# Optimization experiments

Hardware: AMD Instinct MI355X
Metric: run time of the kernel (lower is better)

Reference implementation:

```python
import jax, jax.numpy as jnp
import numpy as np

B, T, I, H, O = 512, 1024, 15, 64, 11

def setup_inputs() -> dict:
    key = jax.random.key(0)
    ks = jax.random.split(key, 7)
    s_ih = 1.0 / np.sqrt(H)
    return {
        "x": jax.random.normal(ks[0], (B, T, I), dtype=jnp.float32),
        # torch nn.RNN params: weight_ih_l0 [H,I], weight_hh_l0 [H,H], biases [H]
        "W_ih": jax.random.uniform(ks[1], (H, I), jnp.float32, -s_ih, s_ih),
        "b_ih": jax.random.uniform(ks[2], (H,), jnp.float32, -s_ih, s_ih),
        "W_hh": jax.random.uniform(ks[3], (H, H), jnp.float32, -s_ih, s_ih),
        "b_hh": jax.random.uniform(ks[4], (H,), jnp.float32, -s_ih, s_ih),
        # decoder Linear(64, 11)
        "W_dec": jax.random.uniform(ks[5], (O, H), jnp.float32, -s_ih, s_ih),
        "b_dec": jax.random.uniform(ks[6], (O,), jnp.float32, -s_ih, s_ih),
    }

def reference(x, W_ih, b_ih, W_hh, b_hh, W_dec, b_dec):
    # Precompute input projection for all timesteps: [T, B, H]
    xproj = jnp.einsum("bti,hi->tbh", x, W_ih) + b_ih + b_hh
    h0 = jnp.zeros((x.shape[0], W_hh.shape[0]), dtype=x.dtype)

    def step(h, xp_t):
        h_new = jax.nn.relu(xp_t + h @ W_hh.T)  # [B, H]
        return h_new, h_new

    h_last, hs = jax.lax.scan(step, h0, xproj)  # hs: [T, B, H]
    out_seq = jnp.transpose(hs, (1, 0, 2))       # [B, T, H]
    out = jax.nn.relu(jnp.einsum("bth,oh->bto", out_seq, W_dec) + b_dec)
    h = h_last[None]  # [1, B, H] matching torch num_layers dim
    return (out, h)
```

## Files before the change

kernel.cpp:

```cpp
#include <hip/hip_runtime.h>
#include <hip/hip_fp16.h>
#include <stdint.h>

#define BB 512
#define TT 1024
#define II 15
#define HH 64
#define OO 11

typedef __fp16 half2v __attribute__((ext_vector_type(2)));
typedef _Float16 half8 __attribute__((ext_vector_type(8)));
typedef float floatx4 __attribute__((ext_vector_type(4)));
typedef int int4v __attribute__((ext_vector_type(4)));

union PK { int i; half2v h; float f; };

__device__ __forceinline__ half2v i2h2(int v) { PK u; u.i = v; return u.h; }
__device__ __forceinline__ int h22i(half2v v) { PK u; u.h = v; return u.i; }

__device__ __forceinline__ float FDOT2(half2v a, half2v b, float c) {
    return __builtin_amdgcn_fdot2(a, b, c, false);
}

__device__ __forceinline__ float lane_xor1(float v) {
    PK u; u.f = v;
    u.i = __builtin_amdgcn_mov_dpp(u.i, 0xB1, 0xF, 0xF, false);
    return u.f;
}

__global__ __launch_bounds__(64) void rnn_rec(
    const float* __restrict__ x, const float* __restrict__ W_ih,
    const float* __restrict__ b_ih, const float* __restrict__ W_hh,
    const float* __restrict__ b_hh, _Float16* __restrict__ hs,
    float* __restrict__ h_last)
{
    __shared__ __align__(16) int xbuf[64 * 8];
    __shared__ __align__(16) int hbuf[64];
    const int b = blockIdx.x;
    const int lane = threadIdx.x;

    half2v whh[32];
#pragma unroll
    for (int j = 0; j < 32; ++j)
        whh[j] = __builtin_amdgcn_cvt_pkrtz(W_hh[lane * HH + 2 * j],
                                            W_hh[lane * HH + 2 * j + 1]);
    half2v wx[8];
#pragma unroll
    for (int j = 0; j < 7; ++j)
        wx[j] = __builtin_amdgcn_cvt_pkrtz(W_ih[lane * II + 2 * j],
                                           W_ih[lane * II + 2 * j + 1]);
    wx[7] = __builtin_amdgcn_cvt_pkrtz(W_ih[lane * II + 14],
                                       b_ih[lane] + b_hh[lane]);

    const float* xb = x + (size_t)b * TT * II;
    _Float16* hrow = hs + (size_t)b * TT * HH + lane;
    const int hwslot = (lane >> 1) | ((lane & 1) << 5);

    {
        float cf[II];
#pragma unroll
        for (int i = 0; i < II; ++i) cf[i] = xb[lane * II + i];
        int4v p0, p1;
        p0.x = h22i(__builtin_amdgcn_cvt_pkrtz(cf[0], cf[1]));
        p0.y = h22i(__builtin_amdgcn_cvt_pkrtz(cf[2], cf[3]));
        p0.z = h22i(__builtin_amdgcn_cvt_pkrtz(cf[4], cf[5]));
        p0.w = h22i(__builtin_amdgcn_cvt_pkrtz(cf[6], cf[7]));
        p1.x = h22i(__builtin_amdgcn_cvt_pkrtz(cf[8], cf[9]));
        p1.y = h22i(__builtin_amdgcn_cvt_pkrtz(cf[10], cf[11]));
        p1.z = h22i(__builtin_amdgcn_cvt_pkrtz(cf[12], cf[13]));
        p1.w = h22i(__builtin_amdgcn_cvt_pkrtz(cf[14], 1.0f));
        *(int4v*)&xbuf[lane * 8] = p0;
        *(int4v*)&xbuf[lane * 8 + 4] = p1;
    }

    float h = 0.0f;

    for (int tc = 0; tc < TT; tc += 64) {
        const int tnb = (tc + 64 < TT) ? (tc + 64) : tc;
        float nf[II];
#pragma unroll
        for (int i = 0; i < II; ++i)
            nf[i] = xb[(size_t)(tnb + lane) * II + i];

#pragma unroll 4
        for (int ts = 0; ts < 64; ++ts) {
            PK hp;
            hp.h = __builtin_amdgcn_cvt_pkrtz(h, lane_xor1(h));
            hbuf[hwslot] = hp.i;

            const int4v xv0 = *(const int4v*)&xbuf[ts * 8];
            const int4v xv1 = *(const int4v*)&xbuf[ts * 8 + 4];
            int4v hb[8];
#pragma unroll
            for (int q = 0; q < 8; ++q)
                hb[q] = *(const int4v*)&hbuf[q * 4];

            float a0 = FDOT2(i2h2(xv0.x), wx[0], 0.0f);
            float a1 = FDOT2(i2h2(xv0.y), wx[1], 0.0f);
            float a2 = FDOT2(i2h2(xv0.z), wx[2], 0.0f);
            float a3 = FDOT2(i2h2(xv0.w), wx[3], 0.0f);
            a0 = FDOT2(i2h2(xv1.x), wx[4], a0);
            a1 = FDOT2(i2h2(xv1.y), wx[5], a1);
            a2 = FDOT2(i2h2(xv1.z), wx[6], a2);
            a3 = FDOT2(i2h2(xv1.w), wx[7], a3);
#pragma unroll
            for (int q = 0; q < 8; ++q) {
                a0 = FDOT2(i2h2(hb[q].x), whh[4 * q + 0], a0);
                a1 = FDOT2(i2h2(hb[q].y), whh[4 * q + 1], a1);
                a2 = FDOT2(i2h2(hb[q].z), whh[4 * q + 2], a2);
                a3 = FDOT2(i2h2(hb[q].w), whh[4 * q + 3], a3);
            }
            h = fmaxf((a0 + a1) + (a2 + a3), 0.0f);
            *hrow = (_Float16)h;
            hrow += HH;
        }

        int4v p0, p1;
        p0.x = h22i(__builtin_amdgcn_cvt_pkrtz(nf[0], nf[1]));
        p0.y = h22i(__builtin_amdgcn_cvt_pkrtz(nf[2], nf[3]));
        p0.z = h22i(__builtin_amdgcn_cvt_pkrtz(nf[4], nf[5]));
        p0.w = h22i(__builtin_amdgcn_cvt_pkrtz(nf[6], nf[7]));
        p1.x = h22i(__builtin_amdgcn_cvt_pkrtz(nf[8], nf[9]));
        p1.y = h22i(__builtin_amdgcn_cvt_pkrtz(nf[10], nf[11]));
        p1.z = h22i(__builtin_amdgcn_cvt_pkrtz(nf[12], nf[13]));
        p1.w = h22i(__builtin_amdgcn_cvt_pkrtz(nf[14], 1.0f));
        *(int4v*)&xbuf[lane * 8] = p0;
        *(int4v*)&xbuf[lane * 8 + 4] = p1;
    }
    h_last[b * HH + lane] = h;
}

__global__ __launch_bounds__(256) void rnn_decode(
    const _Float16* __restrict__ hs, const float* __restrict__ W_dec,
    const float* __restrict__ b_dec, float* __restrict__ out)
{
    __shared__ __align__(16) _Float16 wl[16 * HH];
    const int tid = threadIdx.x;
    for (int i = tid; i < 16 * HH; i += 256)
        wl[i] = (_Float16)((i < OO * HH) ? W_dec[i] : 0.0f);
    __syncthreads();

    const int lane = tid & 63;
    const int wid  = tid >> 6;
    const int col  = lane & 15;
    const int quad = lane >> 4;
    const float bd = (col < OO) ? b_dec[col] : 0.0f;

    half8 bf0 = *(const half8*)&wl[col * HH + quad * 8];
    half8 bf1 = *(const half8*)&wl[col * HH + 32 + quad * 8];

    const size_t tile = (size_t)blockIdx.x * 4 + wid;
    const size_t btb = tile * 16;
    const _Float16* ap = hs + (btb + (size_t)col) * HH + quad * 8;
    half8 a0 = *(const half8*)ap;
    half8 a1 = *(const half8*)(ap + 32);

    floatx4 acc = {0.0f, 0.0f, 0.0f, 0.0f};
    acc = __builtin_amdgcn_mfma_f32_16x16x32_f16(a0, bf0, acc, 0, 0, 0);
    acc = __builtin_amdgcn_mfma_f32_16x16x32_f16(a1, bf1, acc, 0, 0, 0);

    if (col < OO) {
#pragma unroll
        for (int r = 0; r < 4; ++r) {
            const size_t row = btb + (size_t)(quad * 4 + r);
            out[row * OO + col] = fmaxf(acc[r] + bd, 0.0f);
        }
    }
}

extern "C" void kernel_launch(void* const* d_in, const int* in_sizes, int n_in,
                              void* d_out, int out_size, void* d_ws, size_t ws_size,
                              hipStream_t stream) {
    const float* x     = (const float*)d_in[0];
    const float* W_ih  = (const float*)d_in[1];
    const float* b_ih  = (const float*)d_in[2];
    const float* W_hh  = (const float*)d_in[3];
    const float* b_hh  = (const float*)d_in[4];
    const float* W_dec = (const float*)d_in[5];
    const float* b_dec = (const float*)d_in[6];

    float* out    = (float*)d_out;
    float* h_last = out + (size_t)BB * TT * OO;
    _Float16* hs  = (_Float16*)d_ws;

    rnn_rec<<<BB, 64, 0, stream>>>(x, W_ih, b_ih, W_hh, b_hh, hs, h_last);
    rnn_decode<<<8192, 256, 0, stream>>>(hs, W_dec, b_dec, out);
}
```

Before: 276.2 us.

## Fuse decoder into recurrent kernel and drop fp16 hidden-state workspace

Removes the separate MFMA decode kernel and the round trip of all hidden states through global memory. Each timestep now computes the 11 decoder outputs inside the recurrent wavefront, using fdot2 over quarters of h and cross-lane shuffles, and writes them directly. It also changes the shared h buffer to per-lane fp16 writes instead of packed DPP pairs, and splits the recurrence into 8 accumulators for more ILP. The cost is extra LDS reads, shuffles and scattered small stores on the serial critical path of every timestep.

```diff
diff --git a/kernel.cpp b/kernel.cpp
--- a/kernel.cpp
+++ b/kernel.cpp
@@ -9,8 +9,7 @@
 #define OO 11
 
 typedef __fp16 half2v __attribute__((ext_vector_type(2)));
-typedef _Float16 half8 __attribute__((ext_vector_type(8)));
-typedef float floatx4 __attribute__((ext_vector_type(4)));
+typedef int int2v __attribute__((ext_vector_type(2)));
 typedef int int4v __attribute__((ext_vector_type(4)));
 
 union PK { int i; half2v h; float f; };
@@ -22,22 +21,19 @@
     return __builtin_amdgcn_fdot2(a, b, c, false);
 }
 
-__device__ __forceinline__ float lane_xor1(float v) {
-    PK u; u.f = v;
-    u.i = __builtin_amdgcn_mov_dpp(u.i, 0xB1, 0xF, 0xF, false);
-    return u.f;
-}
-
-__global__ __launch_bounds__(64) void rnn_rec(
+__global__ __launch_bounds__(64) void rnn_fused(
     const float* __restrict__ x, const float* __restrict__ W_ih,
     const float* __restrict__ b_ih, const float* __restrict__ W_hh,
-    const float* __restrict__ b_hh, _Float16* __restrict__ hs,
+    const float* __restrict__ b_hh, const float* __restrict__ W_dec,
+    const float* __restrict__ b_dec, float* __restrict__ out,
     float* __restrict__ h_last)
 {
     __shared__ __align__(16) int xbuf[64 * 8];
-    __shared__ __align__(16) int hbuf[64];
+    __shared__ __align__(16) _Float16 hbuf[64];
     const int b = blockIdx.x;
     const int lane = threadIdx.x;
+    const int c = lane & 15;
+    const int g = lane >> 4;
 
     half2v whh[32];
 #pragma unroll
@@ -51,10 +47,17 @@
                                            W_ih[lane * II + 2 * j + 1]);
     wx[7] = __builtin_amdgcn_cvt_pkrtz(W_ih[lane * II + 14],
                                        b_ih[lane] + b_hh[lane]);
+    const int cw = (c < OO) ? c : OO - 1;
+    half2v wd[8];
+#pragma unroll
+    for (int j = 0; j < 8; ++j)
+        wd[j] = __builtin_amdgcn_cvt_pkrtz(W_dec[cw * HH + g * 16 + 2 * j],
+                                           W_dec[cw * HH + g * 16 + 2 * j + 1]);
+    const float bd = b_dec[cw];
+    const bool emit = (g == 0) && (c < OO);
 
     const float* xb = x + (size_t)b * TT * II;
-    _Float16* hrow = hs + (size_t)b * TT * HH + lane;
-    const int hwslot = (lane >> 1) | ((lane & 1) << 5);
+    float* outb = out + (size_t)b * TT * OO;
 
     {
         float cf[II];
@@ -72,6 +75,7 @@
         *(int4v*)&xbuf[lane * 8] = p0;
         *(int4v*)&xbuf[lane * 8 + 4] = p1;
     }
+    hbuf[lane] = (_Float16)0.0f;
 
     float h = 0.0f;
 
@@ -84,35 +88,53 @@
 
 #pragma unroll 4
         for (int ts = 0; ts < 64; ++ts) {
-            PK hp;
-            hp.h = __builtin_amdgcn_cvt_pkrtz(h, lane_xor1(h));
-            hbuf[hwslot] = hp.i;
-
             const int4v xv0 = *(const int4v*)&xbuf[ts * 8];
             const int4v xv1 = *(const int4v*)&xbuf[ts * 8 + 4];
             int4v hb[8];
 #pragma unroll
             for (int q = 0; q < 8; ++q)
-                hb[q] = *(const int4v*)&hbuf[q * 4];
+                hb[q] = *(const int4v*)&hbuf[q * 8];
 
             float a0 = FDOT2(i2h2(xv0.x), wx[0], 0.0f);
             float a1 = FDOT2(i2h2(xv0.y), wx[1], 0.0f);
             float a2 = FDOT2(i2h2(xv0.z), wx[2], 0.0f);
             float a3 = FDOT2(i2h2(xv0.w), wx[3], 0.0f);
-            a0 = FDOT2(i2h2(xv1.x), wx[4], a0);
-            a1 = FDOT2(i2h2(xv1.y), wx[5], a1);
-            a2 = FDOT2(i2h2(xv1.z), wx[6], a2);
-            a3 = FDOT2(i2h2(xv1.w), wx[7], a3);
+            float a4 = FDOT2(i2h2(xv1.x), wx[4], 0.0f);
+            float a5 = FDOT2(i2h2(xv1.y), wx[5], 0.0f);
+            float a6 = FDOT2(i2h2(xv1.z), wx[6], 0.0f);
+            float a7 = FDOT2(i2h2(xv1.w), wx[7], 0.0f);
 #pragma unroll
-            for (int q = 0; q < 8; ++q) {
-                a0 = FDOT2(i2h2(hb[q].x), whh[4 * q + 0], a0);
-                a1 = FDOT2(i2h2(hb[q].y), whh[4 * q + 1], a1);
-                a2 = FDOT2(i2h2(hb[q].z), whh[4 * q + 2], a2);
-                a3 = FDOT2(i2h2(hb[q].w), whh[4 * q + 3], a3);
+            for (int q = 0; q < 4; ++q) {
+                a0 = FDOT2(i2h2(hb[2 * q].x), whh[8 * q + 0], a0);
+                a1 = FDOT2(i2h2(hb[2 * q].y), whh[8 * q + 1], a1);
+                a2 = FDOT2(i2h2(hb[2 * q].z), whh[8 * q + 2], a2);
+                a3 = FDOT2(i2h2(hb[2 * q].w), whh[8 * q + 3], a3);
+                a4 = FDOT2(i2h2(hb[2 * q + 1].x), whh[8 * q + 4], a4);
+                a5 = FDOT2(i2h2(hb[2 * q + 1].y), whh[8 * q + 5], a5);
+                a6 = FDOT2(i2h2(hb[2 * q + 1].z), whh[8 * q + 6], a6);
+                a7 = FDOT2(i2h2(hb[2 * q + 1].w), whh[8 * q + 7], a7);
             }
-            h = fmaxf((a0 + a1) + (a2 + a3), 0.0f);
-            *hrow = (_Float16)h;
-            hrow += HH;
+            h = fmaxf(((a0 + a1) + (a2 + a3)) + ((a4 + a5) + (a6 + a7)), 0.0f);
+
+            hbuf[lane] = (_Float16)h;
+
+            const int2v hd0 = *(const int2v*)&hbuf[g * 16];
+            const int2v hd1 = *(const int2v*)&hbuf[g * 16 + 4];
+            float d0 = FDOT2(i2h2(hd0.x), wd[0], 0.0f);
+            float d1 = FDOT2(i2h2(hd0.y), wd[1], 0.0f);
+            d0 = FDOT2(i2h2(hd1.x), wd[2], d0);
+            d1 = FDOT2(i2h2(hd1.y), wd[3], d1);
+            const int2v hd2 = *(const int2v*)&hbuf[g * 16 + 8];
+            const int2v hd3 = *(const int2v*)&hbuf[g * 16 + 12];
+            d0 = FDOT2(i2h2(hd2.x), wd[4], d0);
+            d1 = FDOT2(i2h2(hd2.y), wd[5], d1);
+            d0 = FDOT2(i2h2(hd3.x), wd[6], d0);
+            d1 = FDOT2(i2h2(hd3.y), wd[7], d1);
+            float d = d0 + d1;
+            d += __shfl_xor(d, 16);
+            d += __shfl_xor(d, 32);
+            if (emit)
+                outb[(size_t)(tc + ts) * OO + c] = fmaxf(d + bd, 0.0f);
         }
 
         int4v p0, p1;
@@ -130,44 +152,6 @@
     h_last[b * HH + lane] = h;
 }
 
-__global__ __launch_bounds__(256) void rnn_decode(
-    const _Float16* __restrict__ hs, const float* __restrict__ W_dec,
-    const float* __restrict__ b_dec, float* __restrict__ out)
-{
-    __shared__ __align__(16) _Float16 wl[16 * HH];
-    const int tid = threadIdx.x;
-    for (int i = tid; i < 16 * HH; i += 256)
-        wl[i] = (_Float16)((i < OO * HH) ? W_dec[i] : 0.0f);
-    __syncthreads();
-
-    const int lane = tid & 63;
-    const int wid  = tid >> 6;
-    const int col  = lane & 15;
-    const int quad = lane >> 4;
-    const float bd = (col < OO) ? b_dec[col] : 0.0f;
-
-    half8 bf0 = *(const half8*)&wl[col * HH + quad * 8];
-    half8 bf1 = *(const half8*)&wl[col * HH + 32 + quad * 8];
-
-    const size_t tile = (size_t)blockIdx.x * 4 + wid;
-    const size_t btb = tile * 16;
-    const _Float16* ap = hs + (btb + (size_t)col) * HH + quad * 8;
-    half8 a0 = *(const half8*)ap;
-    half8 a1 = *(const half8*)(ap + 32);
-
-    floatx4 acc = {0.0f, 0.0f, 0.0f, 0.0f};
-    acc = __builtin_amdgcn_mfma_f32_16x16x32_f16(a0, bf0, acc, 0, 0, 0);
-    acc = __builtin_amdgcn_mfma_f32_16x16x32_f16(a1, bf1, acc, 0, 0, 0);
-
-    if (col < OO) {
-#pragma unroll
-        for (int r = 0; r < 4; ++r) {
-            const size_t row = btb + (size_t)(quad * 4 + r);
-            out[row * OO + col] = fmaxf(acc[r] + bd, 0.0f);
-        }
-    }
-}
-
 extern "C" void kernel_launch(void* const* d_in, const int* in_sizes, int n_in,
                               void* d_out, int out_size, void* d_ws, size_t ws_size,
                               hipStream_t stream) {
@@ -181,8 +165,7 @@
 
     float* out    = (float*)d_out;
     float* h_last = out + (size_t)BB * TT * OO;
-    _Float16* hs  = (_Float16*)d_ws;
 
-    rnn_rec<<<BB, 64, 0, stream>>>(x, W_ih, b_ih, W_hh, b_hh, hs, h_last);
-    rnn_decode<<<8192, 256, 0, stream>>>(hs, W_dec, b_dec, out);
+    rnn_fused<<<BB, 64, 0, stream>>>(x, W_ih, b_ih, W_hh, b_hh,
+                                     W_dec, b_dec, out, h_last);
 }
```

After: 401.5 us. 1.45x slower.

## Pipeline next-step input projection off the recurrent critical path in RNN kernel

Applied to the files above, without the earlier changes.

Restructures the recurrence so the input projection for timestep t+1 is computed right after h_t is produced, while the next hidden-state dot products run, and seeds the accumulators with it. This removes the x-dot-products from the serial dependency chain. The hidden state is now stored as individual fp16 lanes in LDS instead of DPP-packed pairs, which drops the cross-lane move. The x buffer is double-buffered, with the refill placed mid-chunk, and the recurrent dot product uses 8 accumulators instead of 4 to shorten the reduction chain. Costs are more registers and a wider final reduction. Correctness relies on the wavefront executing in lockstep, since the LDS hbuf write and read have no barrier.

```diff
diff --git a/kernel.cpp b/kernel.cpp
--- a/kernel.cpp
+++ b/kernel.cpp
@@ -20,12 +20,6 @@
 
 __device__ __forceinline__ float FDOT2(half2v a, half2v b, float c) {
     return __builtin_amdgcn_fdot2(a, b, c, false);
-}
-
-__device__ __forceinline__ float lane_xor1(float v) {
-    PK u; u.f = v;
-    u.i = __builtin_amdgcn_mov_dpp(u.i, 0xB1, 0xF, 0xF, false);
-    return u.f;
 }
 
 __global__ __launch_bounds__(64) void rnn_rec(
@@ -34,16 +28,16 @@
     const float* __restrict__ b_hh, _Float16* __restrict__ hs,
     float* __restrict__ h_last)
 {
-    __shared__ __align__(16) int xbuf[64 * 8];
-    __shared__ __align__(16) int hbuf[64];
+    __shared__ __align__(16) int xbuf[2][64 * 8];
+    __shared__ __align__(16) _Float16 hbuf[64];
     const int b = blockIdx.x;
     const int lane = threadIdx.x;
 
     half2v whh[32];
 #pragma unroll
-    for (int j = 0; j < 32; ++j)
-        whh[j] = __builtin_amdgcn_cvt_pkrtz(W_hh[lane * HH + 2 * j],
-                                            W_hh[lane * HH + 2 * j + 1]);
+    for (int p = 0; p < 32; ++p)
+        whh[p] = __builtin_amdgcn_cvt_pkrtz(W_hh[lane * HH + 2 * p],
+                                            W_hh[lane * HH + 2 * p + 1]);
     half2v wx[8];
 #pragma unroll
     for (int j = 0; j < 7; ++j)
@@ -54,7 +48,7 @@
 
     const float* xb = x + (size_t)b * TT * II;
     _Float16* hrow = hs + (size_t)b * TT * HH + lane;
-    const int hwslot = (lane >> 1) | ((lane & 1) << 5);
+    const int4v* hb4 = (const int4v*)hbuf;
 
     {
         float cf[II];
@@ -69,11 +63,64 @@
         p1.y = h22i(__builtin_amdgcn_cvt_pkrtz(cf[10], cf[11]));
         p1.z = h22i(__builtin_amdgcn_cvt_pkrtz(cf[12], cf[13]));
         p1.w = h22i(__builtin_amdgcn_cvt_pkrtz(cf[14], 1.0f));
-        *(int4v*)&xbuf[lane * 8] = p0;
-        *(int4v*)&xbuf[lane * 8 + 4] = p1;
+        *(int4v*)&xbuf[0][lane * 8] = p0;
+        *(int4v*)&xbuf[0][lane * 8 + 4] = p1;
+    }
+    hbuf[lane] = (_Float16)0.0f;
+
+    float xa[8];
+    {
+        const int4v xv0 = *(const int4v*)&xbuf[0][0];
+        const int4v xv1 = *(const int4v*)&xbuf[0][4];
+        xa[0] = FDOT2(i2h2(xv0.x), wx[0], 0.0f);
+        xa[1] = FDOT2(i2h2(xv0.y), wx[1], 0.0f);
+        xa[2] = FDOT2(i2h2(xv0.z), wx[2], 0.0f);
+        xa[3] = FDOT2(i2h2(xv0.w), wx[3], 0.0f);
+        xa[4] = FDOT2(i2h2(xv1.x), wx[4], 0.0f);
+        xa[5] = FDOT2(i2h2(xv1.y), wx[5], 0.0f);
+        xa[6] = FDOT2(i2h2(xv1.z), wx[6], 0.0f);
+        xa[7] = FDOT2(i2h2(xv1.w), wx[7], 0.0f);
     }
 
     float h = 0.0f;
+
+    auto step = [&](int t) {
+        int4v hb[8];
+#pragma unroll
+        for (int q = 0; q < 8; ++q) hb[q] = hb4[q];
+
+        const int tn = t + 1;
+        const int* xp = &xbuf[(tn >> 6) & 1][(tn & 63) * 8];
+        const int4v xv0 = *(const int4v*)xp;
+        const int4v xv1 = *(const int4v*)(xp + 4);
+
+        float a0 = xa[0], a1 = xa[1], a2 = xa[2], a3 = xa[3];
+        float a4 = xa[4], a5 = xa[5], a6 = xa[6], a7 = xa[7];
+#pragma unroll
+        for (int r = 0; r < 4; ++r) {
+            a0 = FDOT2(i2h2(hb[2 * r].x),     whh[8 * r + 0], a0);
+            a1 = FDOT2(i2h2(hb[2 * r].y),     whh[8 * r + 1], a1);
+            a2 = FDOT2(i2h2(hb[2 * r].z),     whh[8 * r + 2], a2);
+            a3 = FDOT2(i2h2(hb[2 * r].w),     whh[8 * r + 3], a3);
+            a4 = FDOT2(i2h2(hb[2 * r + 1].x), whh[8 * r + 4], a4);
+            a5 = FDOT2(i2h2(hb[2 * r + 1].y), whh[8 * r + 5], a5);
+            a6 = FDOT2(i2h2(hb[2 * r + 1].z), whh[8 * r + 6], a6);
+            a7 = FDOT2(i2h2(hb[2 * r + 1].w), whh[8 * r + 7], a7);
+        }
+        h = fmaxf(((a0 + a1) + (a2 + a3)) + ((a4 + a5) + (a6 + a7)), 0.0f);
+        const _Float16 hf = (_Float16)h;
+        hbuf[lane] = hf;
+        hrow[(size_t)t * HH] = hf;
+
+        xa[0] = FDOT2(i2h2(xv0.x), wx[0], 0.0f);
+        xa[1] = FDOT2(i2h2(xv0.y), wx[1], 0.0f);
+        xa[2] = FDOT2(i2h2(xv0.z), wx[2], 0.0f);
+        xa[3] = FDOT2(i2h2(xv0.w), wx[3], 0.0f);
+        xa[4] = FDOT2(i2h2(xv1.x), wx[4], 0.0f);
+        xa[5] = FDOT2(i2h2(xv1.y), wx[5], 0.0f);
+        xa[6] = FDOT2(i2h2(xv1.z), wx[6], 0.0f);
+        xa[7] = FDOT2(i2h2(xv1.w), wx[7], 0.0f);
+    };
 
     for (int tc = 0; tc < TT; tc += 64) {
         const int tnb = (tc + 64 < TT) ? (tc + 64) : tc;
@@ -82,50 +129,28 @@
         for (int i = 0; i < II; ++i)
             nf[i] = xb[(size_t)(tnb + lane) * II + i];
 
-#pragma unroll 4
-        for (int ts = 0; ts < 64; ++ts) {
-            PK hp;
-            hp.h = __builtin_amdgcn_cvt_pkrtz(h, lane_xor1(h));
-            hbuf[hwslot] = hp.i;
-
-            const int4v xv0 = *(const int4v*)&xbuf[ts * 8];
-            const int4v xv1 = *(const int4v*)&xbuf[ts * 8 + 4];
-            int4v hb[8];
-#pragma unroll
-            for (int q = 0; q < 8; ++q)
-                hb[q] = *(const int4v*)&hbuf[q * 4];
-
-            float a0 = FDOT2(i2h2(xv0.x), wx[0], 0.0f);
-            float a1 = FDOT2(i2h2(xv0.y), wx[1], 0.0f);
-            float a2 = FDOT2(i2h2(xv0.z), wx[2], 0.0f);
-            float a3 = FDOT2(i2h2(xv0.w), wx[3], 0.0f);
-            a0 = FDOT2(i2h2(xv1.x), wx[4], a0);
-            a1 = FDOT2(i2h2(xv1.y), wx[5], a1);
-            a2 = FDOT2(i2h2(xv1.z), wx[6], a2);
-            a3 = FDOT2(i2h2(xv1.w), wx[7], a3);
-#pragma unroll
-            for (int q = 0; q < 8; ++q) {
-                a0 = FDOT2(i2h2(hb[q].x), whh[4 * q + 0], a0);
-                a1 = FDOT2(i2h2(hb[q].y), whh[4 * q + 1], a1);
-                a2 = FDOT2(i2h2(hb[q].z), whh[4 * q + 2], a2);
-                a3 = FDOT2(i2h2(hb[q].w), whh[4 * q + 3], a3);
-            }
-            h = fmaxf((a0 + a1) + (a2 + a3), 0.0f);
-            *hrow = (_Float16)h;
-            hrow += HH;
+        for (int to = 0; to < 32; to += 8)
+#pragma unroll
+            for (int u = 0; u < 8; ++u) step(tc + to + u);
+
+        {
+            const int cb = ((tc >> 6) + 1) & 1;
+            int4v p0, p1;
+            p0.x = h22i(__builtin_amdgcn_cvt_pkrtz(nf[0], nf[1]));
+            p0.y = h22i(__builtin_amdgcn_cvt_pkrtz(nf[2], nf[3]));
+            p0.z = h22i(__builtin_amdgcn_cvt_pkrtz(nf[4], nf[5]));
+            p0.w = h22i(__builtin_amdgcn_cvt_pkrtz(nf[6], nf[7]));
+            p1.x = h22i(__builtin_amdgcn_cvt_pkrtz(nf[8], nf[9]));
+            p1.y = h22i(__builtin_amdgcn_cvt_pkrtz(nf[10], nf[11]));
+            p1.z = h22i(__builtin_amdgcn_cvt_pkrtz(nf[12], nf[13]));
+            p1.w = h22i(__builtin_amdgcn_cvt_pkrtz(nf[14], 1.0f));
+            *(int4v*)&xbuf[cb][lane * 8] = p0;
+            *(int4v*)&xbuf[cb][lane * 8 + 4] = p1;
         }
 
-        int4v p0, p1;
-        p0.x = h22i(__builtin_amdgcn_cvt_pkrtz(nf[0], nf[1]));
-        p0.y = h22i(__builtin_amdgcn_cvt_pkrtz(nf[2], nf[3]));
-        p0.z = h22i(__builtin_amdgcn_cvt_pkrtz(nf[4], nf[5]));
-        p0.w = h22i(__builtin_amdgcn_cvt_pkrtz(nf[6], nf[7]));
-        p1.x = h22i(__builtin_amdgcn_cvt_pkrtz(nf[8], nf[9]));
-        p1.y = h22i(__builtin_amdgcn_cvt_pkrtz(nf[10], nf[11]));
-        p1.z = h22i(__builtin_amdgcn_cvt_pkrtz(nf[12], nf[13]));
-        p1.w = h22i(__builtin_amdgcn_cvt_pkrtz(nf[14], 1.0f));
-        *(int4v*)&xbuf[lane * 8] = p0;
-        *(int4v*)&xbuf[lane * 8 + 4] = p1;
+        for (int to = 32; to < 64; to += 8)
+#pragma unroll
+            for (int u = 0; u < 8; ++u) step(tc + to + u);
     }
     h_last[b * HH + lane] = h;
 }
```

New measurement: 273.8 us. Within noise of the previous version (-0.9%).
